# Kernel optimization log

Measured on AMD Instinct MI355X. Metric: run time of the kernel, lower is better.

## Reference

```python
import jax, jax.numpy as jnp
import numpy as np

N, L, D, HEADS = 32, 128, 128, 4
B = 64
MHSA_RESIDUAL = False  # module default


def setup_inputs() -> dict:
    key = jax.random.key(0)
    ks = jax.random.split(key, 21)
    g = lambda k, shape, s=0.05: jax.random.normal(k, shape, dtype=jnp.float32) * s
    return {
        "X": jax.random.normal(ks[0], (B, L, N), dtype=jnp.float32),
        # per-variable encoder LSTM weights, stacked over N (torch gate order i,f,g,o)
        "enc_Wih": g(ks[1], (N, 4 * D)),        # input size is 1 -> (4d,1) squeezed
        "enc_Whh": g(ks[2], (N, 4 * D, D)),
        "enc_bih": g(ks[3], (N, 4 * D)),
        "enc_bhh": g(ks[4], (N, 4 * D)),
        "pool_w": g(ks[5], (N, D)),
        "pool_b": g(ks[6], (N,)),
        # nn.MultiheadAttention packed in-proj + out-proj
        "Wqkv": g(ks[7], (3 * D, D)),
        "bqkv": g(ks[8], (3 * D,)),
        "Wo": g(ks[9], (D, D)),
        "bo": g(ks[10], (D,)),
        # per-variable decoder: init_h/init_c Linear(d, d), LSTM, out Linear(d,1)
        "dec_ih_W": g(ks[11], (N, D, D)),
        "dec_ih_b": g(ks[12], (N, D)),
        "dec_ic_W": g(ks[13], (N, D, D)),
        "dec_ic_b": g(ks[14], (N, D)),
        "dec_Wih": g(ks[15], (N, 4 * D)),       # unused at runtime: decoder input is zeros
        "dec_Whh": g(ks[16], (N, 4 * D, D)),
        "dec_bih": g(ks[17], (N, 4 * D)),
        "dec_bhh": g(ks[18], (N, 4 * D)),
        "dec_out_W": g(ks[19], (N, D)),
        "dec_out_b": g(ks[20], (N,)),
    }


def _lstm_cell(pre, c):
    i, f, g, o = jnp.split(pre, 4, axis=-1)
    c_new = jax.nn.sigmoid(f) * c + jax.nn.sigmoid(i) * jnp.tanh(g)
    h_new = jax.nn.sigmoid(o) * jnp.tanh(c_new)
    return h_new, c_new


def reference(X, enc_Wih, enc_Whh, enc_bih, enc_bhh, pool_w, pool_b,
              Wqkv, bqkv, Wo, bo,
              dec_ih_W, dec_ih_b, dec_ic_W, dec_ic_b,
              dec_Wih, dec_Whh, dec_bih, dec_bhh, dec_out_W, dec_out_b):
    Bx = X.shape[0]
    # ---- N per-variable LSTM encoders, batched over the N axis ----
    x_enc = jnp.transpose(X[:, :L - 1, :], (1, 2, 0))  # (L-1, N, B)
    h0 = jnp.zeros((N, Bx, D), X.dtype)

    def enc_step(carry, x_t):
        h, c = carry
        pre = (x_t[..., None] * enc_Wih[:, None, :]
               + jnp.einsum('nbd,ngd->nbg', h, enc_Whh)
               + (enc_bih + enc_bhh)[:, None, :])
        h, c = _lstm_cell(pre, c)
        return (h, c), h

    _, H = jax.lax.scan(enc_step, (h0, h0), x_enc)  # (L-1, N, B, D)

    # temporal attention pooling (softmax over time)
    s = jnp.einsum('tnbd,nd->tnb', H, pool_w) + pool_b[None, :, None]
    a = jax.nn.softmax(s, axis=0)
    C = jnp.transpose(jnp.einsum('tnb,tnbd->nbd', a, H), (1, 0, 2))  # (B, N, D)

    # ---- MHSA over the variable axis ----
    qkv = C @ Wqkv.T + bqkv  # (B, N, 3D)
    q, k, v = jnp.split(qkv, 3, axis=-1)
    dh = D // HEADS
    split = lambda t: t.reshape(Bx, N, HEADS, dh).transpose(0, 2, 1, 3)  # (B,h,N,dh)
    q, k, v = split(q), split(k), split(v)
    attn = jax.nn.softmax(jnp.einsum('bhqd,bhkd->bhqk', q, k) / jnp.sqrt(jnp.float32(dh)), axis=-1)
    A = jnp.einsum('bhqk,bhkd->bhqd', attn, v).transpose(0, 2, 1, 3).reshape(Bx, N, D)
    A = A @ Wo.T + bo
    C_star = C + A if MHSA_RESIDUAL else A  # (B, N, D)

    # ---- N per-variable LSTM decoders, batched over the N axis ----
    cs = jnp.transpose(C_star, (1, 0, 2))  # (N, B, D)
    h = jnp.tanh(jnp.einsum('nbd,ned->nbe', cs, dec_ih_W) + dec_ih_b[:, None, :])
    c = jnp.tanh(jnp.einsum('nbd,ned->nbe', cs, dec_ic_W) + dec_ic_b[:, None, :])

    def dec_step(carry, _):
        h, c = carry
        # decoder input is identically zero -> W_ih contributes nothing
        pre = jnp.einsum('nbd,ngd->nbg', h, dec_Whh) + (dec_bih + dec_bhh)[:, None, :]
        h, c = _lstm_cell(pre, c)
        return (h, c), h

    _, Y = jax.lax.scan(dec_step, (h, c), None, length=L)  # (L, N, B, D)
    O = jnp.einsum('lnbd,nd->lnb', Y, dec_out_W) + dec_out_b[None, :, None]  # (L, N, B)
    recon = jnp.transpose(O[:L - 1], (2, 0, 1))  # (B, L-1, N)
    pred = O[L - 1].T                             # (B, N)
    return recon, pred, C_star
```

## Files before the change

### kernel.cpp

```cpp
#include <hip/hip_runtime.h>


typedef _Float16 h8  __attribute__((ext_vector_type(8)));
typedef _Float16 h4v __attribute__((ext_vector_type(4)));
typedef float    f4  __attribute__((ext_vector_type(4)));
typedef float    f2v __attribute__((ext_vector_type(2)));

#define DI __device__ __forceinline__

constexpr int NV  = 32;
constexpr int LT  = 128;
constexpr int DH  = 128;
constexpr int GG  = 4 * DH;
constexpr int BR  = 8;
constexpr int NW  = 8;
constexpr int TPB = NW * 64;
constexpr int HSTR = DH + 8;
constexpr float LOG2E = 1.4426950408889634f;

DI float rcp_(float x) { return __builtin_amdgcn_rcpf(x); }
DI float ex2_(float x) { return __builtin_amdgcn_exp2f(x); }

DI float tanh_(float x) {
    float xc = fminf(fmaxf(x, -20.0f), 20.0f);
    float E = ex2_(2.0f * LOG2E * xc);
    return (E - 1.0f) * rcp_(E + 1.0f);
}

DI float lstm_cell(float iv, float fv, float gv, float ov, float& c) {
    float Ai = ex2_(iv);
    float Af = ex2_(fv);
    float Bg = ex2_(gv);
    float ai1 = 1.0f + Ai, af1 = 1.0f + Af, bg1 = 1.0f + Bg;
    float P = ai1 * bg1;
    float N = fmaf(c, P, (Bg - 1.0f) * af1);
    c = N * rcp_(P * af1);
    float cc = fminf(fmaxf(c, -20.0f), 20.0f);
    float Ec = ex2_(2.0f * LOG2E * cc);
    float Eo = ex2_(ov);
    return (Ec - 1.0f) * rcp_((1.0f + Eo) * (1.0f + Ec));
}

DI h8 cvt8(f4 a, f4 b) {
    h8 r;
    r[0] = (_Float16)a[0]; r[1] = (_Float16)a[1];
    r[2] = (_Float16)a[2]; r[3] = (_Float16)a[3];
    r[4] = (_Float16)b[0]; r[5] = (_Float16)b[1];
    r[6] = (_Float16)b[2]; r[7] = (_Float16)b[3];
    return r;
}
DI h8 cvt8s(f4 a, f4 b, float s) {
    h8 r;
    r[0] = (_Float16)(a[0] * s); r[1] = (_Float16)(a[1] * s);
    r[2] = (_Float16)(a[2] * s); r[3] = (_Float16)(a[3] * s);
    r[4] = (_Float16)(b[0] * s); r[5] = (_Float16)(b[1] * s);
    r[6] = (_Float16)(b[2] * s); r[7] = (_Float16)(b[3] * s);
    return r;
}

__constant__ float GSC[4] = {-LOG2E, -LOG2E, 2.0f * LOG2E, -LOG2E};

__global__ __launch_bounds__(TPB, 2)
void enc_kernel(const float* __restrict__ X,
                const float* __restrict__ Wih,
                const float* __restrict__ Whh,
                const float* __restrict__ bih,
                const float* __restrict__ bhh,
                const float* __restrict__ poolw,
                float* __restrict__ Cout)
{
    const int n    = blockIdx.x & 31;
    const int b0   = (blockIdx.x >> 5) * BR;
    const int tid  = threadIdx.x;
    const int wv   = tid >> 6;
    const int lane = tid & 63;
    const int quad = lane >> 4;
    const int l16  = lane & 15;
    const int dmy  = wv * 16 + l16;

    __shared__ _Float16 hbuf[2][16 * HSTR];
    __shared__ float xs[(LT - 1) * BR];
    __shared__ float pfin[2][BR];

    h8 Wf[4][4];
    float wihr[4];
    f4 bsp[4];
#pragma unroll
    for (int g4 = 0; g4 < 4; ++g4) {
        const float s = GSC[g4];
        const int g = g4 * DH + dmy;
        const float* wrow = Whh + (size_t)(n * GG + g) * DH;
#pragma unroll
        for (int kc = 0; kc < 4; ++kc) {
            f4 w0 = *(const f4*)(wrow + kc * 32 + quad * 8);
            f4 w1 = *(const f4*)(wrow + kc * 32 + quad * 8 + 4);
            Wf[g4][kc] = cvt8s(w0, w1, s);
        }
        wihr[g4] = Wih[n * GG + g] * s;
        const float bb = (bih[n * GG + g] + bhh[n * GG + g]) * s;
        bsp[g4] = (f4){bb, bb, bb, bb};
    }
    h8 Bp[4];
#pragma unroll
    for (int kc = 0; kc < 4; ++kc) {
        if (l16 == 0) {
            f4 p0 = *(const f4*)(poolw + n * DH + kc * 32 + quad * 8);
            f4 p1 = *(const f4*)(poolw + n * DH + kc * 32 + quad * 8 + 4);
            Bp[kc] = cvt8s(p0, p1, LOG2E);
        } else {
            Bp[kc] = (h8)(_Float16)0.0f;
        }
    }

    for (int i = tid; i < (LT - 1) * BR; i += TPB)
        xs[i] = X[((size_t)(b0 + (i & 7)) * LT + (i >> 3)) * NV + n];
    for (int i = tid; i < 2 * 16 * HSTR; i += TPB)
        ((_Float16*)hbuf)[i] = (_Float16)0.0f;
    __syncthreads();

    float cst[2]   = {0.f, 0.f};
    float lsum[2]  = {0.f, 0.f};
    float acc[2]   = {0.f, 0.f};
    float hprev[2] = {0.f, 0.f};

    for (int t = 0; t < LT - 1; ++t) {
        const _Float16* hb = hbuf[t & 1];
        h8 a[4];
#pragma unroll
        for (int kc = 0; kc < 4; ++kc)
            a[kc] = *(const h8*)(hb + l16 * HSTR + kc * 32 + quad * 8);

        f4 pre[4];
#pragma unroll
        for (int g4 = 0; g4 < 4; ++g4)
            pre[g4] = __builtin_amdgcn_mfma_f32_16x16x32_f16(
                a[0], Wf[g4][0], bsp[g4], 0, 0, 0);
#pragma unroll
        for (int kc = 1; kc < 4; ++kc)
#pragma unroll
            for (int g4 = 0; g4 < 4; ++g4)
                pre[g4] = __builtin_amdgcn_mfma_f32_16x16x32_f16(
                    a[kc], Wf[g4][kc], pre[g4], 0, 0, 0);

        if (wv == 0) {
            f4 sp = {0.f, 0.f, 0.f, 0.f};
#pragma unroll
            for (int kc = 0; kc < 4; ++kc)
                sp = __builtin_amdgcn_mfma_f32_16x16x32_f16(a[kc], Bp[kc], sp, 0, 0, 0);
            if (l16 == 0) {
                pfin[t & 1][quad * 2 + 0] = ex2_(sp[0]);
                pfin[t & 1][quad * 2 + 1] = ex2_(sp[1]);
            }
        }

        const f2v xv = *(const f2v*)(xs + t * BR + quad * 2);
        float hv[2];
#pragma unroll
        for (int r = 0; r < 2; ++r) {
            hv[r] = lstm_cell(fmaf(xv[r], wihr[0], pre[0][r]),
                              fmaf(xv[r], wihr[1], pre[1][r]),
                              fmaf(xv[r], wihr[2], pre[2][r]),
                              fmaf(xv[r], wihr[3], pre[3][r]), cst[r]);
        }

        _Float16* hn = hbuf[(t + 1) & 1];
#pragma unroll
        for (int r = 0; r < 2; ++r)
            hn[(quad * 4 + r) * HSTR + dmy] = (_Float16)hv[r];
        __syncthreads();

        if (t > 0) {
#pragma unroll
            for (int r = 0; r < 2; ++r) {
                const float p = pfin[t & 1][quad * 2 + r];
                lsum[r] += p;
                acc[r] = fmaf(p, hprev[r], acc[r]);
            }
        }
#pragma unroll
        for (int r = 0; r < 2; ++r) hprev[r] = hv[r];
    }

    if (wv == 0) {
        const _Float16* hb = hbuf[(LT - 1) & 1];
        h8 a[4];
#pragma unroll
        for (int kc = 0; kc < 4; ++kc)
            a[kc] = *(const h8*)(hb + l16 * HSTR + kc * 32 + quad * 8);
        f4 sp = {0.f, 0.f, 0.f, 0.f};
#pragma unroll
        for (int kc = 0; kc < 4; ++kc)
            sp = __builtin_amdgcn_mfma_f32_16x16x32_f16(a[kc], Bp[kc], sp, 0, 0, 0);
        if (l16 == 0) {
            pfin[(LT - 1) & 1][quad * 2 + 0] = ex2_(sp[0]);
            pfin[(LT - 1) & 1][quad * 2 + 1] = ex2_(sp[1]);
        }
    }
    __syncthreads();
#pragma unroll
    for (int r = 0; r < 2; ++r) {
        const float p = pfin[(LT - 1) & 1][quad * 2 + r];
        lsum[r] += p;
        acc[r] = fmaf(p, hprev[r], acc[r]);
    }
#pragma unroll
    for (int r = 0; r < 2; ++r) {
        const int b = b0 + quad * 2 + r;
        Cout[((size_t)b * NV + n) * DH + dmy] = acc[r] * rcp_(lsum[r]);
    }
}

constexpr int CS2 = DH + 8;
constexpr int QS  = 40;

__global__ __launch_bounds__(256)
void attn_kernel(const float* __restrict__ Cin,
                 const float* __restrict__ Wqkv,
                 const float* __restrict__ bqkv,
                 float* __restrict__ Astage)
{
    const int b    = blockIdx.x >> 2;
    const int hh   = blockIdx.x & 3;
    const int tid  = threadIdx.x;
    const int wv   = tid >> 6;
    const int lane = tid & 63;
    const int quad = lane >> 4;
    const int l16  = lane & 15;

    __shared__ _Float16 Cb[NV][CS2];
    __shared__ _Float16 qs[NV][QS], ks[NV][QS], vT[NV][QS];
    __shared__ float    S[NV][NV + 1];
    __shared__ _Float16 P[NV][QS];

    for (int i = tid; i < NV * DH / 4; i += 256) {
        const int nn = i >> 5, d4 = (i & 31) * 4;
        f4 v = *(const f4*)(Cin + ((size_t)b * NV + nn) * DH + d4);
        h4v hv4;
        hv4[0] = (_Float16)v[0]; hv4[1] = (_Float16)v[1];
        hv4[2] = (_Float16)v[2]; hv4[3] = (_Float16)v[3];
        *(h4v*)(&Cb[nn][d4]) = hv4;
    }
    __syncthreads();

    const int m0 = (wv >> 1) * 16;
    const int n0 = (wv & 1) * 16;

    h8 a[4];
#pragma unroll
    for (int kc = 0; kc < 4; ++kc)
        a[kc] = *(const h8*)(&Cb[m0 + l16][kc * 32 + quad * 8]);

#pragma unroll
    for (int mat = 0; mat < 3; ++mat) {
        const int rbase = mat * DH + hh * 32;
        const float* wrow = Wqkv + (size_t)(rbase + n0 + l16) * DH;
        const float bias  = bqkv[rbase + n0 + l16];
        f4 acc = {bias, bias, bias, bias};
#pragma unroll
        for (int kc = 0; kc < 4; ++kc) {
            f4 w0 = *(const f4*)(wrow + kc * 32 + quad * 8);
            f4 w1 = *(const f4*)(wrow + kc * 32 + quad * 8 + 4);
            acc = __builtin_amdgcn_mfma_f32_16x16x32_f16(a[kc], cvt8(w0, w1), acc, 0, 0, 0);
        }
#pragma unroll
        for (int r = 0; r < 4; ++r) {
            const int tok = m0 + quad * 4 + r, col = n0 + l16;
            if (mat == 0)      qs[tok][col] = (_Float16)acc[r];
            else if (mat == 1) ks[tok][col] = (_Float16)acc[r];
            else               vT[col][tok] = (_Float16)acc[r];
        }
    }
    __syncthreads();

    {
        h8 aq = *(const h8*)(&qs[m0 + l16][quad * 8]);
        h8 bk = *(const h8*)(&ks[n0 + l16][quad * 8]);
        f4 sc = {0.f, 0.f, 0.f, 0.f};
        sc = __builtin_amdgcn_mfma_f32_16x16x32_f16(aq, bk, sc, 0, 0, 0);
#pragma unroll
        for (int r = 0; r < 4; ++r)
            S[m0 + quad * 4 + r][n0 + l16] = sc[r] * 0.17677669529663687f;
    }
    __syncthreads();

    if (tid < NV) {
        float mx = -1e30f;
        for (int j = 0; j < NV; ++j) mx = fmaxf(mx, S[tid][j]);
        float l = 0.0f;
        float p[NV];
#pragma unroll
        for (int j = 0; j < NV; ++j) {
            p[j] = ex2_(LOG2E * (S[tid][j] - mx));
            l += p[j];
        }
        const float rl = rcp_(l);
#pragma unroll
        for (int j = 0; j < NV; ++j) P[tid][j] = (_Float16)(p[j] * rl);
    }
    __syncthreads();

    {
        h8 ap = *(const h8*)(&P[m0 + l16][quad * 8]);
        h8 bv = *(const h8*)(&vT[n0 + l16][quad * 8]);
        f4 av = {0.f, 0.f, 0.f, 0.f};
        av = __builtin_amdgcn_mfma_f32_16x16x32_f16(ap, bv, av, 0, 0, 0);
#pragma unroll
        for (int r = 0; r < 4; ++r) {
            const int tok = m0 + quad * 4 + r;
            Astage[((size_t)b * NV + tok) * DH + hh * 32 + n0 + l16] = av[r];
        }
    }
}

__global__ __launch_bounds__(256)
void outproj_kernel(const float* __restrict__ Wo,
                    const float* __restrict__ bo,
                    float* __restrict__ AC)
{
    const int mb   = blockIdx.x * 16;
    const int tid  = threadIdx.x;
    const int wv   = tid >> 6;
    const int lane = tid & 63;
    const int quad = lane >> 4;
    const int l16  = lane & 15;

    __shared__ _Float16 As[16][HSTR];

    for (int i = tid; i < 16 * DH / 4; i += 256) {
        const int rr = i >> 5, d4 = (i & 31) * 4;
        f4 v = *(const f4*)(AC + ((size_t)(mb + rr)) * DH + d4);
        h4v hv4;
        hv4[0] = (_Float16)v[0]; hv4[1] = (_Float16)v[1];
        hv4[2] = (_Float16)v[2]; hv4[3] = (_Float16)v[3];
        *(h4v*)(&As[rr][d4]) = hv4;
    }
    __syncthreads();

    h8 a[4];
#pragma unroll
    for (int kc = 0; kc < 4; ++kc)
        a[kc] = *(const h8*)(&As[l16][kc * 32 + quad * 8]);

#pragma unroll
    for (int i = 0; i < 2; ++i) {
        const int n0 = (wv * 2 + i) * 16;
        const float* wrow = Wo + (size_t)(n0 + l16) * DH;
        const float bias  = bo[n0 + l16];
        f4 acc = {bias, bias, bias, bias};
#pragma unroll
        for (int kc = 0; kc < 4; ++kc) {
            f4 w0 = *(const f4*)(wrow + kc * 32 + quad * 8);
            f4 w1 = *(const f4*)(wrow + kc * 32 + quad * 8 + 4);
            acc = __builtin_amdgcn_mfma_f32_16x16x32_f16(a[kc], cvt8(w0, w1), acc, 0, 0, 0);
        }
#pragma unroll
        for (int r = 0; r < 4; ++r)
            AC[((size_t)(mb + quad * 4 + r)) * DH + n0 + l16] = acc[r];
    }
}

__global__ __launch_bounds__(TPB, 2)
void dec_kernel(const float* __restrict__ Cstar,
                const float* __restrict__ ihW,
                const float* __restrict__ ihb,
                const float* __restrict__ icW,
                const float* __restrict__ icb,
                const float* __restrict__ Whh,
                const float* __restrict__ bih,
                const float* __restrict__ bhh,
                const float* __restrict__ outW,
                const float* __restrict__ outb,
                float* __restrict__ recon,
                float* __restrict__ pred)
{
    const int n    = blockIdx.x & 31;
    const int b0   = (blockIdx.x >> 5) * BR;
    const int tid  = threadIdx.x;
    const int wv   = tid >> 6;
    const int lane = tid & 63;
    const int quad = lane >> 4;
    const int l16  = lane & 15;
    const int dmy  = wv * 16 + l16;

    __shared__ _Float16 hbuf[2][16 * HSTR];
    __shared__ float obuf[LT - 1][BR];

    h8 Wf[4][4];
    f4 bsp[4];
#pragma unroll
    for (int g4 = 0; g4 < 4; ++g4) {
        const float s = GSC[g4];
        const int g = g4 * DH + dmy;
        const float* wrow = Whh + (size_t)(n * GG + g) * DH;
#pragma unroll
        for (int kc = 0; kc < 4; ++kc) {
            f4 w0 = *(const f4*)(wrow + kc * 32 + quad * 8);
            f4 w1 = *(const f4*)(wrow + kc * 32 + quad * 8 + 4);
            Wf[g4][kc] = cvt8s(w0, w1, s);
        }
        const float bb = (bih[n * GG + g] + bhh[n * GG + g]) * s;
        bsp[g4] = (f4){bb, bb, bb, bb};
    }
    h8 Bo[4];
#pragma unroll
    for (int kc = 0; kc < 4; ++kc) {
        if (l16 == 0) {
            f4 p0 = *(const f4*)(outW + n * DH + kc * 32 + quad * 8);
            f4 p1 = *(const f4*)(outW + n * DH + kc * 32 + quad * 8 + 4);
            Bo[kc] = cvt8(p0, p1);
        } else {
            Bo[kc] = (h8)(_Float16)0.0f;
        }
    }
    const float ob = outb[n];

    for (int i = tid; i < 2 * 16 * HSTR; i += TPB)
        ((_Float16*)hbuf)[i] = (_Float16)0.0f;
    __syncthreads();
    if (tid < 256) {
        const int j = tid >> 5, d4 = (tid & 31) * 4;
        const int row = (j >> 1) * 4 + (j & 1);
        f4 v = *(const f4*)(Cstar + ((size_t)(b0 + j) * NV + n) * DH + d4);
        h4v hv4;
        hv4[0] = (_Float16)v[0]; hv4[1] = (_Float16)v[1];
        hv4[2] = (_Float16)v[2]; hv4[3] = (_Float16)v[3];
        *(h4v*)(&hbuf[0][row * HSTR + d4]) = hv4;
    }
    __syncthreads();

    float cst[2], hv0[2];
    {
        h8 a[4];
#pragma unroll
        for (int kc = 0; kc < 4; ++kc)
            a[kc] = *(const h8*)(hbuf[0] + l16 * HSTR + kc * 32 + quad * 8);
        const float bh = ihb[n * DH + dmy];
        const float bc = icb[n * DH + dmy];
        f4 Ph = {bh, bh, bh, bh};
        f4 Pc = {bc, bc, bc, bc};
        const float* hrow = ihW + (size_t)(n * DH + dmy) * DH;
        const float* crow = icW + (size_t)(n * DH + dmy) * DH;
#pragma unroll
        for (int kc = 0; kc < 4; ++kc) {
            f4 w0 = *(const f4*)(hrow + kc * 32 + quad * 8);
            f4 w1 = *(const f4*)(hrow + kc * 32 + quad * 8 + 4);
            Ph = __builtin_amdgcn_mfma_f32_16x16x32_f16(a[kc], cvt8(w0, w1), Ph, 0, 0, 0);
            f4 u0 = *(const f4*)(crow + kc * 32 + quad * 8);
            f4 u1 = *(const f4*)(crow + kc * 32 + quad * 8 + 4);
            Pc = __builtin_amdgcn_mfma_f32_16x16x32_f16(a[kc], cvt8(u0, u1), Pc, 0, 0, 0);
        }
#pragma unroll
        for (int r = 0; r < 2; ++r) {
            hv0[r] = tanh_(Ph[r]);
            cst[r] = tanh_(Pc[r]);
        }
    }
    __syncthreads();
#pragma unroll
    for (int r = 0; r < 2; ++r)
        hbuf[0][(quad * 4 + r) * HSTR + dmy] = (_Float16)hv0[r];
    __syncthreads();

    for (int t = 0; t < LT; ++t) {
        const _Float16* hb = hbuf[t & 1];
        h8 a[4];
#pragma unroll
        for (int kc = 0; kc < 4; ++kc)
            a[kc] = *(const h8*)(hb + l16 * HSTR + kc * 32 + quad * 8);

        f4 pre[4];
#pragma unroll
        for (int g4 = 0; g4 < 4; ++g4)
            pre[g4] = __builtin_amdgcn_mfma_f32_16x16x32_f16(
                a[0], Wf[g4][0], bsp[g4], 0, 0, 0);
#pragma unroll
        for (int kc = 1; kc < 4; ++kc)
#pragma unroll
            for (int g4 = 0; g4 < 4; ++g4)
                pre[g4] = __builtin_amdgcn_mfma_f32_16x16x32_f16(
                    a[kc], Wf[g4][kc], pre[g4], 0, 0, 0);

        if (wv == 0 && t > 0) {
            f4 so = {0.f, 0.f, 0.f, 0.f};
#pragma unroll
            for (int kc = 0; kc < 4; ++kc)
                so = __builtin_amdgcn_mfma_f32_16x16x32_f16(a[kc], Bo[kc], so, 0, 0, 0);
            if (l16 == 0) {
                obuf[t - 1][quad * 2 + 0] = so[0] + ob;
                obuf[t - 1][quad * 2 + 1] = so[1] + ob;
            }
        }

        float hv[2];
#pragma unroll
        for (int r = 0; r < 2; ++r)
            hv[r] = lstm_cell(pre[0][r], pre[1][r], pre[2][r], pre[3][r], cst[r]);

        _Float16* hn = hbuf[(t + 1) & 1];
#pragma unroll
        for (int r = 0; r < 2; ++r)
            hn[(quad * 4 + r) * HSTR + dmy] = (_Float16)hv[r];
        __syncthreads();
    }

    if (wv == 0) {
        const _Float16* hb = hbuf[LT & 1];
        h8 a[4];
#pragma unroll
        for (int kc = 0; kc < 4; ++kc)
            a[kc] = *(const h8*)(hb + l16 * HSTR + kc * 32 + quad * 8);
        f4 so = {0.f, 0.f, 0.f, 0.f};
#pragma unroll
        for (int kc = 0; kc < 4; ++kc)
            so = __builtin_amdgcn_mfma_f32_16x16x32_f16(a[kc], Bo[kc], so, 0, 0, 0);
        if (l16 == 0) {
            pred[(size_t)(b0 + quad * 2 + 0) * NV + n] = so[0] + ob;
            pred[(size_t)(b0 + quad * 2 + 1) * NV + n] = so[1] + ob;
        }
    }

    if (tid < LT - 1) {
#pragma unroll
        for (int b = 0; b < BR; ++b)
            recon[((size_t)(b0 + b) * (LT - 1) + tid) * NV + n] = obuf[tid][b];
    }
}

extern "C" void kernel_launch(void* const* d_in, const int* in_sizes, int n_in,
                              void* d_out, int out_size, void* d_ws, size_t ws_size,
                              hipStream_t stream) {
    (void)in_sizes; (void)n_in; (void)d_ws; (void)ws_size; (void)out_size;

    const float* X     = (const float*)d_in[0];
    const float* eWih  = (const float*)d_in[1];
    const float* eWhh  = (const float*)d_in[2];
    const float* ebih  = (const float*)d_in[3];
    const float* ebhh  = (const float*)d_in[4];
    const float* poolw = (const float*)d_in[5];
    const float* Wqkv  = (const float*)d_in[7];
    const float* bqkv  = (const float*)d_in[8];
    const float* Wo    = (const float*)d_in[9];
    const float* bo    = (const float*)d_in[10];
    const float* dihW  = (const float*)d_in[11];
    const float* dihb  = (const float*)d_in[12];
    const float* dicW  = (const float*)d_in[13];
    const float* dicb  = (const float*)d_in[14];
    const float* dWhh  = (const float*)d_in[16];
    const float* dbih  = (const float*)d_in[17];
    const float* dbhh  = (const float*)d_in[18];
    const float* doutW = (const float*)d_in[19];
    const float* doutb = (const float*)d_in[20];

    float* out   = (float*)d_out;
    float* recon = out;
    float* pred  = out + 64 * 127 * 32;
    float* Cstar = out + 64 * 127 * 32 + 64 * 32;
    float* Cpool = out;

    enc_kernel<<<dim3(256), dim3(TPB), 0, stream>>>(
        X, eWih, eWhh, ebih, ebhh, poolw, Cpool);
    attn_kernel<<<dim3(256), dim3(256), 0, stream>>>(
        Cpool, Wqkv, bqkv, Cstar);
    outproj_kernel<<<dim3(128), dim3(256), 0, stream>>>(
        Wo, bo, Cstar);
    dec_kernel<<<dim3(256), dim3(TPB), 0, stream>>>(
        Cstar, dihW, dihb, dicW, dicb, dWhh, dbih, dbhh,
        doutW, doutb, recon, pred);
}
```

Baseline: 292.8 us.

## Fuse out-projection into decoder and split per-step pooling MFMAs across waves

Removes the separate out-projection kernel. The decoder now reads the attention output, applies Wo and bo itself, writes C_star, and feeds the result straight into its init-state GEMM. The per-timestep pooling-score and output-projection MFMA chains, which wave 0 used to run alone, are split so four waves each do one MFMA; the partial sums go through a small shared buffer and are added by the consumers. A-fragment LDS reads for the unused padding rows are redirected to a shared row, which cuts LDS traffic. The cost is extra shared-memory reduction reads and writes each step, plus Wo loads in every decoder block.

```diff
diff --git a/kernel.cpp b/kernel.cpp
--- a/kernel.cpp
+++ b/kernel.cpp
@@ -77,10 +77,11 @@
     const int quad = lane >> 4;
     const int l16  = lane & 15;
     const int dmy  = wv * 16 + l16;
+    const int rowA = ((l16 & 3) < 2) ? l16 : 2;
 
     __shared__ _Float16 hbuf[2][16 * HSTR];
     __shared__ float xs[(LT - 1) * BR];
-    __shared__ float pfin[2][BR];
+    __shared__ float sred[2][BR][4];
 
     h8 Wf[4][4];
     float wihr[4];
@@ -100,17 +101,13 @@
         const float bb = (bih[n * GG + g] + bhh[n * GG + g]) * s;
         bsp[g4] = (f4){bb, bb, bb, bb};
     }
-    h8 Bp[4];
-#pragma unroll
-    for (int kc = 0; kc < 4; ++kc) {
-        if (l16 == 0) {
-            f4 p0 = *(const f4*)(poolw + n * DH + kc * 32 + quad * 8);
-            f4 p1 = *(const f4*)(poolw + n * DH + kc * 32 + quad * 8 + 4);
-            Bp[kc] = cvt8s(p0, p1, LOG2E);
-        } else {
-            Bp[kc] = (h8)(_Float16)0.0f;
-        }
-    }
+    h8 Bp = (h8)(_Float16)0.0f;
+    if (wv < 4 && l16 == 0) {
+        f4 p0 = *(const f4*)(poolw + n * DH + wv * 32 + quad * 8);
+        f4 p1 = *(const f4*)(poolw + n * DH + wv * 32 + quad * 8 + 4);
+        Bp = cvt8s(p0, p1, LOG2E);
+    }
+    const f4 z4 = {0.f, 0.f, 0.f, 0.f};
 
     for (int i = tid; i < (LT - 1) * BR; i += TPB)
         xs[i] = X[((size_t)(b0 + (i & 7)) * LT + (i >> 3)) * NV + n];
@@ -124,11 +121,11 @@
     float hprev[2] = {0.f, 0.f};
 
     for (int t = 0; t < LT - 1; ++t) {
-        const _Float16* hb = hbuf[t & 1];
+        const _Float16* ab = hbuf[t & 1] + rowA * HSTR + quad * 8;
         h8 a[4];
 #pragma unroll
         for (int kc = 0; kc < 4; ++kc)
-            a[kc] = *(const h8*)(hb + l16 * HSTR + kc * 32 + quad * 8);
+            a[kc] = *(const h8*)(ab + kc * 32);
 
         f4 pre[4];
 #pragma unroll
@@ -142,14 +139,11 @@
                 pre[g4] = __builtin_amdgcn_mfma_f32_16x16x32_f16(
                     a[kc], Wf[g4][kc], pre[g4], 0, 0, 0);
 
-        if (wv == 0) {
-            f4 sp = {0.f, 0.f, 0.f, 0.f};
-#pragma unroll
-            for (int kc = 0; kc < 4; ++kc)
-                sp = __builtin_amdgcn_mfma_f32_16x16x32_f16(a[kc], Bp[kc], sp, 0, 0, 0);
+        if (wv < 4) {
+            f4 sp = __builtin_amdgcn_mfma_f32_16x16x32_f16(a[wv], Bp, z4, 0, 0, 0);
             if (l16 == 0) {
-                pfin[t & 1][quad * 2 + 0] = ex2_(sp[0]);
-                pfin[t & 1][quad * 2 + 1] = ex2_(sp[1]);
+                sred[t & 1][quad * 2 + 0][wv] = sp[0];
+                sred[t & 1][quad * 2 + 1][wv] = sp[1];
             }
         }
 
@@ -172,7 +166,8 @@
         if (t > 0) {
 #pragma unroll
             for (int r = 0; r < 2; ++r) {
-                const float p = pfin[t & 1][quad * 2 + r];
+                const f4 s4 = *(const f4*)&sred[t & 1][quad * 2 + r][0];
+                const float p = ex2_((s4[0] + s4[1]) + (s4[2] + s4[3]));
                 lsum[r] += p;
                 acc[r] = fmaf(p, hprev[r], acc[r]);
             }
@@ -181,25 +176,19 @@
         for (int r = 0; r < 2; ++r) hprev[r] = hv[r];
     }
 
-    if (wv == 0) {
-        const _Float16* hb = hbuf[(LT - 1) & 1];
-        h8 a[4];
-#pragma unroll
-        for (int kc = 0; kc < 4; ++kc)
-            a[kc] = *(const h8*)(hb + l16 * HSTR + kc * 32 + quad * 8);
-        f4 sp = {0.f, 0.f, 0.f, 0.f};
-#pragma unroll
-        for (int kc = 0; kc < 4; ++kc)
-            sp = __builtin_amdgcn_mfma_f32_16x16x32_f16(a[kc], Bp[kc], sp, 0, 0, 0);
+    if (wv < 4) {
+        h8 at = *(const h8*)(hbuf[(LT - 1) & 1] + rowA * HSTR + wv * 32 + quad * 8);
+        f4 sp = __builtin_amdgcn_mfma_f32_16x16x32_f16(at, Bp, z4, 0, 0, 0);
         if (l16 == 0) {
-            pfin[(LT - 1) & 1][quad * 2 + 0] = ex2_(sp[0]);
-            pfin[(LT - 1) & 1][quad * 2 + 1] = ex2_(sp[1]);
+            sred[(LT - 1) & 1][quad * 2 + 0][wv] = sp[0];
+            sred[(LT - 1) & 1][quad * 2 + 1][wv] = sp[1];
         }
     }
     __syncthreads();
 #pragma unroll
     for (int r = 0; r < 2; ++r) {
-        const float p = pfin[(LT - 1) & 1][quad * 2 + r];
+        const f4 s4 = *(const f4*)&sred[(LT - 1) & 1][quad * 2 + r][0];
+        const float p = ex2_((s4[0] + s4[1]) + (s4[2] + s4[3]));
         lsum[r] += p;
         acc[r] = fmaf(p, hprev[r], acc[r]);
     }
@@ -312,55 +301,11 @@
     }
 }
 
-__global__ __launch_bounds__(256)
-void outproj_kernel(const float* __restrict__ Wo,
-                    const float* __restrict__ bo,
-                    float* __restrict__ AC)
-{
-    const int mb   = blockIdx.x * 16;
-    const int tid  = threadIdx.x;
-    const int wv   = tid >> 6;
-    const int lane = tid & 63;
-    const int quad = lane >> 4;
-    const int l16  = lane & 15;
-
-    __shared__ _Float16 As[16][HSTR];
-
-    for (int i = tid; i < 16 * DH / 4; i += 256) {
-        const int rr = i >> 5, d4 = (i & 31) * 4;
-        f4 v = *(const f4*)(AC + ((size_t)(mb + rr)) * DH + d4);
-        h4v hv4;
-        hv4[0] = (_Float16)v[0]; hv4[1] = (_Float16)v[1];
-        hv4[2] = (_Float16)v[2]; hv4[3] = (_Float16)v[3];
-        *(h4v*)(&As[rr][d4]) = hv4;
-    }
-    __syncthreads();
-
-    h8 a[4];
-#pragma unroll
-    for (int kc = 0; kc < 4; ++kc)
-        a[kc] = *(const h8*)(&As[l16][kc * 32 + quad * 8]);
-
-#pragma unroll
-    for (int i = 0; i < 2; ++i) {
-        const int n0 = (wv * 2 + i) * 16;
-        const float* wrow = Wo + (size_t)(n0 + l16) * DH;
-        const float bias  = bo[n0 + l16];
-        f4 acc = {bias, bias, bias, bias};
-#pragma unroll
-        for (int kc = 0; kc < 4; ++kc) {
-            f4 w0 = *(const f4*)(wrow + kc * 32 + quad * 8);
-            f4 w1 = *(const f4*)(wrow + kc * 32 + quad * 8 + 4);
-            acc = __builtin_amdgcn_mfma_f32_16x16x32_f16(a[kc], cvt8(w0, w1), acc, 0, 0, 0);
-        }
-#pragma unroll
-        for (int r = 0; r < 4; ++r)
-            AC[((size_t)(mb + quad * 4 + r)) * DH + n0 + l16] = acc[r];
-    }
-}
-
 __global__ __launch_bounds__(TPB, 2)
-void dec_kernel(const float* __restrict__ Cstar,
+void dec_kernel(const float* __restrict__ A,
+                float* __restrict__ Cst,
+                const float* __restrict__ Wo,
+                const float* __restrict__ bo,
                 const float* __restrict__ ihW,
                 const float* __restrict__ ihb,
                 const float* __restrict__ icW,
@@ -381,9 +326,11 @@
     const int quad = lane >> 4;
     const int l16  = lane & 15;
     const int dmy  = wv * 16 + l16;
+    const int rowA = ((l16 & 3) < 2) ? l16 : 2;
 
     __shared__ _Float16 hbuf[2][16 * HSTR];
     __shared__ float obuf[LT - 1][BR];
+    __shared__ float sred[2][BR][4];
 
     h8 Wf[4][4];
     f4 bsp[4];
@@ -401,18 +348,14 @@
         const float bb = (bih[n * GG + g] + bhh[n * GG + g]) * s;
         bsp[g4] = (f4){bb, bb, bb, bb};
     }
-    h8 Bo[4];
-#pragma unroll
-    for (int kc = 0; kc < 4; ++kc) {
-        if (l16 == 0) {
-            f4 p0 = *(const f4*)(outW + n * DH + kc * 32 + quad * 8);
-            f4 p1 = *(const f4*)(outW + n * DH + kc * 32 + quad * 8 + 4);
-            Bo[kc] = cvt8(p0, p1);
-        } else {
-            Bo[kc] = (h8)(_Float16)0.0f;
-        }
+    h8 Bo = (h8)(_Float16)0.0f;
+    if (wv < 4 && l16 == 0) {
+        f4 p0 = *(const f4*)(outW + n * DH + wv * 32 + quad * 8);
+        f4 p1 = *(const f4*)(outW + n * DH + wv * 32 + quad * 8 + 4);
+        Bo = cvt8(p0, p1);
     }
     const float ob = outb[n];
+    const f4 z4 = {0.f, 0.f, 0.f, 0.f};
 
     for (int i = tid; i < 2 * 16 * HSTR; i += TPB)
         ((_Float16*)hbuf)[i] = (_Float16)0.0f;
@@ -420,7 +363,7 @@
     if (tid < 256) {
         const int j = tid >> 5, d4 = (tid & 31) * 4;
         const int row = (j >> 1) * 4 + (j & 1);
-        f4 v = *(const f4*)(Cstar + ((size_t)(b0 + j) * NV + n) * DH + d4);
+        f4 v = *(const f4*)(A + ((size_t)(b0 + j) * NV + n) * DH + d4);
         h4v hv4;
         hv4[0] = (_Float16)v[0]; hv4[1] = (_Float16)v[1];
         hv4[2] = (_Float16)v[2]; hv4[3] = (_Float16)v[3];
@@ -428,12 +371,37 @@
     }
     __syncthreads();
 
+    {
+        const _Float16* ab = hbuf[0] + rowA * HSTR + quad * 8;
+        h8 a[4];
+#pragma unroll
+        for (int kc = 0; kc < 4; ++kc)
+            a[kc] = *(const h8*)(ab + kc * 32);
+        const float bias = bo[dmy];
+        f4 acc = {bias, bias, bias, bias};
+        const float* wrow = Wo + (size_t)dmy * DH;
+#pragma unroll
+        for (int kc = 0; kc < 4; ++kc) {
+            f4 w0 = *(const f4*)(wrow + kc * 32 + quad * 8);
+            f4 w1 = *(const f4*)(wrow + kc * 32 + quad * 8 + 4);
+            acc = __builtin_amdgcn_mfma_f32_16x16x32_f16(a[kc], cvt8(w0, w1), acc, 0, 0, 0);
+        }
+        __syncthreads();
+#pragma unroll
+        for (int r = 0; r < 2; ++r) {
+            hbuf[1][(quad * 4 + r) * HSTR + dmy] = (_Float16)acc[r];
+            Cst[((size_t)(b0 + quad * 2 + r) * NV + n) * DH + dmy] = acc[r];
+        }
+    }
+    __syncthreads();
+
     float cst[2], hv0[2];
     {
+        const _Float16* ab = hbuf[1] + rowA * HSTR + quad * 8;
         h8 a[4];
 #pragma unroll
         for (int kc = 0; kc < 4; ++kc)
-            a[kc] = *(const h8*)(hbuf[0] + l16 * HSTR + kc * 32 + quad * 8);
+            a[kc] = *(const h8*)(ab + kc * 32);
         const float bh = ihb[n * DH + dmy];
         const float bc = icb[n * DH + dmy];
         f4 Ph = {bh, bh, bh, bh};
@@ -462,11 +430,11 @@
     __syncthreads();
 
     for (int t = 0; t < LT; ++t) {
-        const _Float16* hb = hbuf[t & 1];
+        const _Float16* ab = hbuf[t & 1] + rowA * HSTR + quad * 8;
         h8 a[4];
 #pragma unroll
         for (int kc = 0; kc < 4; ++kc)
-            a[kc] = *(const h8*)(hb + l16 * HSTR + kc * 32 + quad * 8);
+            a[kc] = *(const h8*)(ab + kc * 32);
 
         f4 pre[4];
 #pragma unroll
@@ -480,14 +448,11 @@
                 pre[g4] = __builtin_amdgcn_mfma_f32_16x16x32_f16(
                     a[kc], Wf[g4][kc], pre[g4], 0, 0, 0);
 
-        if (wv == 0 && t > 0) {
-            f4 so = {0.f, 0.f, 0.f, 0.f};
-#pragma unroll
-            for (int kc = 0; kc < 4; ++kc)
-                so = __builtin_amdgcn_mfma_f32_16x16x32_f16(a[kc], Bo[kc], so, 0, 0, 0);
+        if (wv < 4) {
+            f4 so = __builtin_amdgcn_mfma_f32_16x16x32_f16(a[wv], Bo, z4, 0, 0, 0);
             if (l16 == 0) {
-                obuf[t - 1][quad * 2 + 0] = so[0] + ob;
-                obuf[t - 1][quad * 2 + 1] = so[1] + ob;
+                sred[t & 1][quad * 2 + 0][wv] = so[0];
+                sred[t & 1][quad * 2 + 1][wv] = so[1];
             }
         }
 
@@ -501,22 +466,25 @@
         for (int r = 0; r < 2; ++r)
             hn[(quad * 4 + r) * HSTR + dmy] = (_Float16)hv[r];
         __syncthreads();
-    }
-
-    if (wv == 0) {
-        const _Float16* hb = hbuf[LT & 1];
-        h8 a[4];
-#pragma unroll
-        for (int kc = 0; kc < 4; ++kc)
-            a[kc] = *(const h8*)(hb + l16 * HSTR + kc * 32 + quad * 8);
-        f4 so = {0.f, 0.f, 0.f, 0.f};
-#pragma unroll
-        for (int kc = 0; kc < 4; ++kc)
-            so = __builtin_amdgcn_mfma_f32_16x16x32_f16(a[kc], Bo[kc], so, 0, 0, 0);
+
+        if (t > 0 && tid < BR) {
+            const f4 s4 = *(const f4*)&sred[t & 1][tid][0];
+            obuf[t - 1][tid] = (s4[0] + s4[1]) + (s4[2] + s4[3]) + ob;
+        }
+    }
+
+    if (wv < 4) {
+        h8 at = *(const h8*)(hbuf[LT & 1] + rowA * HSTR + wv * 32 + quad * 8);
+        f4 so = __builtin_amdgcn_mfma_f32_16x16x32_f16(at, Bo, z4, 0, 0, 0);
         if (l16 == 0) {
-            pred[(size_t)(b0 + quad * 2 + 0) * NV + n] = so[0] + ob;
-            pred[(size_t)(b0 + quad * 2 + 1) * NV + n] = so[1] + ob;
-        }
+            sred[LT & 1][quad * 2 + 0][wv] = so[0];
+            sred[LT & 1][quad * 2 + 1][wv] = so[1];
+        }
+    }
+    __syncthreads();
+    if (tid < BR) {
+        const f4 s4 = *(const f4*)&sred[LT & 1][tid][0];
+        pred[(size_t)(b0 + tid) * NV + n] = (s4[0] + s4[1]) + (s4[2] + s4[3]) + ob;
     }
 
     if (tid < LT - 1) {
@@ -556,14 +524,13 @@
     float* pred  = out + 64 * 127 * 32;
     float* Cstar = out + 64 * 127 * 32 + 64 * 32;
     float* Cpool = out;
+    float* Astg  = Cstar;
 
     enc_kernel<<<dim3(256), dim3(TPB), 0, stream>>>(
         X, eWih, eWhh, ebih, ebhh, poolw, Cpool);
     attn_kernel<<<dim3(256), dim3(256), 0, stream>>>(
-        Cpool, Wqkv, bqkv, Cstar);
-    outproj_kernel<<<dim3(128), dim3(256), 0, stream>>>(
-        Wo, bo, Cstar);
+        Cpool, Wqkv, bqkv, Astg);
     dec_kernel<<<dim3(256), dim3(TPB), 0, stream>>>(
-        Cstar, dihW, dihb, dicW, dicb, dWhh, dbih, dbhh,
+        Astg, Cstar, Wo, bo, dihW, dihb, dicW, dicb, dWhh, dbih, dbhh,
         doutW, doutb, recon, pred);
 }
```

Result: slower. 694.5 us (+137.1%).

## Fuse attention out-projection into decoder kernel and remap padded MFMA A-rows

Applied to the files above, without the earlier changes.

Removes the separate outproj kernel launch: the decoder kernel now loads the raw attention output, applies Wo/bo with MFMA per block, writes C_star to global memory, and feeds it from LDS into the init_h/init_c projections. The A-operand row index for the 16-row MFMA tile is remapped so padded rows alias valid rows (rowA), which changes the LDS read addresses in the recurrent loops. The aim is to save one launch and a global round trip, at the cost of each decoder block redundantly loading Wo. A and Cst alias the same buffer, but each block reads its own rows before writing them, with a barrier in between.

```diff
diff --git a/kernel.cpp b/kernel.cpp
--- a/kernel.cpp
+++ b/kernel.cpp
@@ -77,6 +77,7 @@
     const int quad = lane >> 4;
     const int l16  = lane & 15;
     const int dmy  = wv * 16 + l16;
+    const int rowA = ((l16 & 3) < 2) ? l16 : 2;
 
     __shared__ _Float16 hbuf[2][16 * HSTR];
     __shared__ float xs[(LT - 1) * BR];
@@ -124,11 +125,11 @@
     float hprev[2] = {0.f, 0.f};
 
     for (int t = 0; t < LT - 1; ++t) {
-        const _Float16* hb = hbuf[t & 1];
+        const _Float16* ab = hbuf[t & 1] + rowA * HSTR + quad * 8;
         h8 a[4];
 #pragma unroll
         for (int kc = 0; kc < 4; ++kc)
-            a[kc] = *(const h8*)(hb + l16 * HSTR + kc * 32 + quad * 8);
+            a[kc] = *(const h8*)(ab + kc * 32);
 
         f4 pre[4];
 #pragma unroll
@@ -182,11 +183,11 @@
     }
 
     if (wv == 0) {
-        const _Float16* hb = hbuf[(LT - 1) & 1];
+        const _Float16* ab = hbuf[(LT - 1) & 1] + rowA * HSTR + quad * 8;
         h8 a[4];
 #pragma unroll
         for (int kc = 0; kc < 4; ++kc)
-            a[kc] = *(const h8*)(hb + l16 * HSTR + kc * 32 + quad * 8);
+            a[kc] = *(const h8*)(ab + kc * 32);
         f4 sp = {0.f, 0.f, 0.f, 0.f};
 #pragma unroll
         for (int kc = 0; kc < 4; ++kc)
@@ -312,55 +313,11 @@
     }
 }
 
-__global__ __launch_bounds__(256)
-void outproj_kernel(const float* __restrict__ Wo,
-                    const float* __restrict__ bo,
-                    float* __restrict__ AC)
-{
-    const int mb   = blockIdx.x * 16;
-    const int tid  = threadIdx.x;
-    const int wv   = tid >> 6;
-    const int lane = tid & 63;
-    const int quad = lane >> 4;
-    const int l16  = lane & 15;
-
-    __shared__ _Float16 As[16][HSTR];
-
-    for (int i = tid; i < 16 * DH / 4; i += 256) {
-        const int rr = i >> 5, d4 = (i & 31) * 4;
-        f4 v = *(const f4*)(AC + ((size_t)(mb + rr)) * DH + d4);
-        h4v hv4;
-        hv4[0] = (_Float16)v[0]; hv4[1] = (_Float16)v[1];
-        hv4[2] = (_Float16)v[2]; hv4[3] = (_Float16)v[3];
-        *(h4v*)(&As[rr][d4]) = hv4;
-    }
-    __syncthreads();
-
-    h8 a[4];
-#pragma unroll
-    for (int kc = 0; kc < 4; ++kc)
-        a[kc] = *(const h8*)(&As[l16][kc * 32 + quad * 8]);
-
-#pragma unroll
-    for (int i = 0; i < 2; ++i) {
-        const int n0 = (wv * 2 + i) * 16;
-        const float* wrow = Wo + (size_t)(n0 + l16) * DH;
-        const float bias  = bo[n0 + l16];
-        f4 acc = {bias, bias, bias, bias};
-#pragma unroll
-        for (int kc = 0; kc < 4; ++kc) {
-            f4 w0 = *(const f4*)(wrow + kc * 32 + quad * 8);
-            f4 w1 = *(const f4*)(wrow + kc * 32 + quad * 8 + 4);
-            acc = __builtin_amdgcn_mfma_f32_16x16x32_f16(a[kc], cvt8(w0, w1), acc, 0, 0, 0);
-        }
-#pragma unroll
-        for (int r = 0; r < 4; ++r)
-            AC[((size_t)(mb + quad * 4 + r)) * DH + n0 + l16] = acc[r];
-    }
-}
-
 __global__ __launch_bounds__(TPB, 2)
-void dec_kernel(const float* __restrict__ Cstar,
+void dec_kernel(const float* __restrict__ A,
+                float* __restrict__ Cst,
+                const float* __restrict__ Wo,
+                const float* __restrict__ bo,
                 const float* __restrict__ ihW,
                 const float* __restrict__ ihb,
                 const float* __restrict__ icW,
@@ -381,6 +338,7 @@
     const int quad = lane >> 4;
     const int l16  = lane & 15;
     const int dmy  = wv * 16 + l16;
+    const int rowA = ((l16 & 3) < 2) ? l16 : 2;
 
     __shared__ _Float16 hbuf[2][16 * HSTR];
     __shared__ float obuf[LT - 1][BR];
@@ -420,7 +378,7 @@
     if (tid < 256) {
         const int j = tid >> 5, d4 = (tid & 31) * 4;
         const int row = (j >> 1) * 4 + (j & 1);
-        f4 v = *(const f4*)(Cstar + ((size_t)(b0 + j) * NV + n) * DH + d4);
+        f4 v = *(const f4*)(A + ((size_t)(b0 + j) * NV + n) * DH + d4);
         h4v hv4;
         hv4[0] = (_Float16)v[0]; hv4[1] = (_Float16)v[1];
         hv4[2] = (_Float16)v[2]; hv4[3] = (_Float16)v[3];
@@ -428,12 +386,37 @@
     }
     __syncthreads();
 
+    {
+        const _Float16* ab = hbuf[0] + rowA * HSTR + quad * 8;
+        h8 a[4];
+#pragma unroll
+        for (int kc = 0; kc < 4; ++kc)
+            a[kc] = *(const h8*)(ab + kc * 32);
+        const float bias = bo[dmy];
+        f4 acc = {bias, bias, bias, bias};
+        const float* wrow = Wo + (size_t)dmy * DH;
+#pragma unroll
+        for (int kc = 0; kc < 4; ++kc) {
+            f4 w0 = *(const f4*)(wrow + kc * 32 + quad * 8);
+            f4 w1 = *(const f4*)(wrow + kc * 32 + quad * 8 + 4);
+            acc = __builtin_amdgcn_mfma_f32_16x16x32_f16(a[kc], cvt8(w0, w1), acc, 0, 0, 0);
+        }
+        __syncthreads();
+#pragma unroll
+        for (int r = 0; r < 2; ++r) {
+            hbuf[1][(quad * 4 + r) * HSTR + dmy] = (_Float16)acc[r];
+            Cst[((size_t)(b0 + quad * 2 + r) * NV + n) * DH + dmy] = acc[r];
+        }
+    }
+    __syncthreads();
+
     float cst[2], hv0[2];
     {
+        const _Float16* ab = hbuf[1] + rowA * HSTR + quad * 8;
         h8 a[4];
 #pragma unroll
         for (int kc = 0; kc < 4; ++kc)
-            a[kc] = *(const h8*)(hbuf[0] + l16 * HSTR + kc * 32 + quad * 8);
+            a[kc] = *(const h8*)(ab + kc * 32);
         const float bh = ihb[n * DH + dmy];
         const float bc = icb[n * DH + dmy];
         f4 Ph = {bh, bh, bh, bh};
@@ -462,11 +445,11 @@
     __syncthreads();
 
     for (int t = 0; t < LT; ++t) {
-        const _Float16* hb = hbuf[t & 1];
+        const _Float16* ab = hbuf[t & 1] + rowA * HSTR + quad * 8;
         h8 a[4];
 #pragma unroll
         for (int kc = 0; kc < 4; ++kc)
-            a[kc] = *(const h8*)(hb + l16 * HSTR + kc * 32 + quad * 8);
+            a[kc] = *(const h8*)(ab + kc * 32);
 
         f4 pre[4];
 #pragma unroll
@@ -504,11 +487,11 @@
     }
 
     if (wv == 0) {
-        const _Float16* hb = hbuf[LT & 1];
+        const _Float16* ab = hbuf[LT & 1] + rowA * HSTR + quad * 8;
         h8 a[4];
 #pragma unroll
         for (int kc = 0; kc < 4; ++kc)
-            a[kc] = *(const h8*)(hb + l16 * HSTR + kc * 32 + quad * 8);
+            a[kc] = *(const h8*)(ab + kc * 32);
         f4 so = {0.f, 0.f, 0.f, 0.f};
 #pragma unroll
         for (int kc = 0; kc < 4; ++kc)
@@ -556,14 +539,13 @@
     float* pred  = out + 64 * 127 * 32;
     float* Cstar = out + 64 * 127 * 32 + 64 * 32;
     float* Cpool = out;
+    float* Astg  = Cstar;
 
     enc_kernel<<<dim3(256), dim3(TPB), 0, stream>>>(
         X, eWih, eWhh, ebih, ebhh, poolw, Cpool);
     attn_kernel<<<dim3(256), dim3(256), 0, stream>>>(
-        Cpool, Wqkv, bqkv, Cstar);
-    outproj_kernel<<<dim3(128), dim3(256), 0, stream>>>(
-        Wo, bo, Cstar);
+        Cpool, Wqkv, bqkv, Astg);
     dec_kernel<<<dim3(256), dim3(TPB), 0, stream>>>(
-        Cstar, dihW, dihb, dicW, dicb, dWhh, dbih, dbhh,
+        Astg, Cstar, Wo, bo, dihW, dihb, dicW, dicb, dWhh, dbih, dbhh,
         doutW, doutb, recon, pred);
 }
```

Result: no change. 292.6 us (-0.1%).
